# Kernel optimization log

Measured on AMD Instinct MI355X. Metric: run time of the kernel, lower is better.

Reference implementation:

```python
import jax, jax.numpy as jnp
import numpy as np

TEMPERATURE = 0.1
NEG_INF = -1e9
EPS = 1e-12

def setup_inputs() -> dict:
    key = jax.random.key(0)
    k1, k2, k3 = jax.random.split(key, 3)
    B, C, H, W = 8, 256, 128, 128
    num_classes = 150
    features = jax.random.normal(k1, (B, C, H, W), dtype=jnp.float32)
    labels = jax.random.randint(k2, (B, H, W), 0, num_classes, dtype=jnp.int32)
    text_embeddings = jax.random.normal(k3, (num_classes, C), dtype=jnp.float32)
    return {"features": features, "labels": labels, "text_embeddings": text_embeddings, "ignore_index": 255}

def _l2_normalize(x, axis=-1):
    n = jnp.linalg.norm(x, axis=axis, keepdims=True)
    return x / jnp.maximum(n, EPS)

def reference(features, labels, text_embeddings, ignore_index):
    num_classes, C = text_embeddings.shape
    B = features.shape[0]
    # [B,C,H,W] -> [B*H*W, C]
    f = jnp.transpose(features, (0, 2, 3, 1)).reshape(-1, C)
    lab = jnp.where(labels == ignore_index, 0, labels).reshape(-1)
    # segment-mean per class (fused scatter-add instead of per-class loop)
    sums = jax.ops.segment_sum(f, lab, num_segments=num_classes)          # [K,C]
    counts = jax.ops.segment_sum(jnp.ones_like(lab, dtype=f.dtype), lab, num_segments=num_classes)  # [K]
    valid = counts > 0
    prototypes = jnp.where(valid[:, None], sums / jnp.maximum(counts, 1.0)[:, None], 0.0)
    prototypes = _l2_normalize(prototypes)
    text_n = _l2_normalize(text_embeddings)
    sim = (prototypes @ text_n.T) / TEMPERATURE                            # [K,K]
    # cross-entropy restricted to valid rows/cols with identity soft targets
    masked = jnp.where(valid[None, :], sim, NEG_INF)                       # mask invalid cols
    logp = jax.nn.log_softmax(masked, axis=-1)
    diag = jnp.diagonal(logp)
    per_row = jnp.where(valid, -diag, 0.0)
    n_valid = jnp.sum(valid.astype(f.dtype))
    loss = jnp.sum(per_row) / jnp.maximum(n_valid, 1.0)
    return jnp.where(n_valid > 1, loss, 0.0)
```

## Files before the change

### kernel.cpp

```cpp
#include <hip/hip_runtime.h>
#include <math.h>

#define EPSV 1e-12f

typedef __attribute__((ext_vector_type(8))) short short8;
typedef __attribute__((ext_vector_type(4))) float f32x4;

constexpr int MT    = 10;
constexpr int K_PAD = 160;
constexpr int CPB   = 64;
constexpr int CHPX  = 64;
constexpr int PBPX  = 1024;
constexpr int NCHK  = PBPX / CHPX;
constexpr int NPB   = 128;
constexpr int THR   = 512;

__global__ __launch_bounds__(THR, 4) void protomm_kernel(
    const float* __restrict__ feat,
    const int*   __restrict__ labels,
    const int*   __restrict__ ign_p,
    float*       __restrict__ partial,
    float*       __restrict__ vmask,
    int C, int HW)
{
    __shared__ float stage[4][4096];
    __shared__ int   labL[PBPX];
    __shared__ unsigned char pres[K_PAD];

    const int tid   = threadIdx.x;
    const int w     = tid >> 6;
    const int lane  = tid & 63;
    const int rowid = lane & 15;
    const int g     = lane >> 4;
    const int ctg   = w & 1;
    const int mg    = w >> 1;

    const int bid = blockIdx.x;
    const int cg  = bid & 3;
    const int pb  = bid >> 2;
    const int b   = pb >> 4;
    const int px0 = (pb & 15) * PBPX;
    const int ig  = *ign_p;

    if (cg == 0)
        for (int i = tid; i < K_PAD; i += THR) pres[i] = 0;
    {
        int l0 = labels[(size_t)b * HW + px0 + tid];
        int l1 = labels[(size_t)b * HW + px0 + THR + tid];
        labL[tid]       = (l0 == ig) ? 0 : l0;
        labL[tid + THR] = (l1 == ig) ? 0 : l1;
    }
    __syncthreads();
    if (cg == 0) {
        int la = labL[tid];
        if ((unsigned)la < (unsigned)K_PAD) pres[la] = 1;
        la = labL[tid + THR];
        if ((unsigned)la < (unsigned)K_PAD) pres[la] = 1;
    }

    const int sch = tid >> 4;
    const int p40 = (tid & 15) ^ (sch & 7);
    const float* gb0 = feat + ((size_t)(b * C + cg * CPB + sch)) * HW + px0 + 4 * p40;
    const float* gb1 = gb0 + (size_t)32 * HW;

    auto ISSUE = [&](int ck) {
        const int buf = ck & 3;
        __builtin_amdgcn_global_load_lds(
            (const __attribute__((address_space(1))) void*)(gb0 + ck * CHPX),
            (__attribute__((address_space(3))) void*)&stage[buf][tid * 4], 16, 0, 0);
        __builtin_amdgcn_global_load_lds(
            (const __attribute__((address_space(1))) void*)(gb1 + ck * CHPX),
            (__attribute__((address_space(3))) void*)&stage[buf][tid * 4 + 2048], 16, 0, 0);
    };

    f32x4 acc0[3], acc1[3];
    #pragma unroll
    for (int j = 0; j < 3; ++j) {
        acc0[j] = (f32x4){0.f, 0.f, 0.f, 0.f};
        acc1[j] = (f32x4){0.f, 0.f, 0.f, 0.f};
    }

    auto CONSUME = [&](int ck) {
        const int buf = ck & 3;
        #pragma unroll
        for (int ks = 0; ks < 2; ++ks) {
            const int pxb = ck * CHPX + ks * 32 + g * 8;
            const int4 lA = *reinterpret_cast<const int4*>(&labL[pxb]);
            const int4 lB = *reinterpret_cast<const int4*>(&labL[pxb + 4]);
            const int px4 = ks * 8 + g * 2;
            short8 bfr0, bfr1;
            {
                const int ch = ctg * 32 + rowid;
                const int x  = ch & 7;
                const float4 f0 = *reinterpret_cast<const float4*>(
                    &stage[buf][(ch * 16 + (px4 ^ x)) * 4]);
                const float4 f1 = *reinterpret_cast<const float4*>(
                    &stage[buf][(ch * 16 + ((px4 + 1) ^ x)) * 4]);
                unsigned q0, q1, q2, q3;
                asm("v_cvt_pk_bf16_f32 %0, %1, %2" : "=v"(q0) : "v"(f0.x), "v"(f0.y));
                asm("v_cvt_pk_bf16_f32 %0, %1, %2" : "=v"(q1) : "v"(f0.z), "v"(f0.w));
                asm("v_cvt_pk_bf16_f32 %0, %1, %2" : "=v"(q2) : "v"(f1.x), "v"(f1.y));
                asm("v_cvt_pk_bf16_f32 %0, %1, %2" : "=v"(q3) : "v"(f1.z), "v"(f1.w));
                bfr0 = __builtin_bit_cast(short8, make_uint4(q0, q1, q2, q3));
            }
            {
                const int ch = ctg * 32 + 16 + rowid;
                const int x  = ch & 7;
                const float4 f0 = *reinterpret_cast<const float4*>(
                    &stage[buf][(ch * 16 + (px4 ^ x)) * 4]);
                const float4 f1 = *reinterpret_cast<const float4*>(
                    &stage[buf][(ch * 16 + ((px4 + 1) ^ x)) * 4]);
                unsigned q0, q1, q2, q3;
                asm("v_cvt_pk_bf16_f32 %0, %1, %2" : "=v"(q0) : "v"(f0.x), "v"(f0.y));
                asm("v_cvt_pk_bf16_f32 %0, %1, %2" : "=v"(q1) : "v"(f0.z), "v"(f0.w));
                asm("v_cvt_pk_bf16_f32 %0, %1, %2" : "=v"(q2) : "v"(f1.x), "v"(f1.y));
                asm("v_cvt_pk_bf16_f32 %0, %1, %2" : "=v"(q3) : "v"(f1.z), "v"(f1.w));
                bfr1 = __builtin_bit_cast(short8, make_uint4(q0, q1, q2, q3));
            }
            #pragma unroll
            for (int j = 0; j < 3; ++j) {
                const int m = mg + 4 * j;
                if (m < MT) {
                    const int tgt = m * 16 + rowid;
                    unsigned a0 = (lA.x == tgt ? 0x3F80u : 0u) | (lA.y == tgt ? 0x3F800000u : 0u);
                    unsigned a1 = (lA.z == tgt ? 0x3F80u : 0u) | (lA.w == tgt ? 0x3F800000u : 0u);
                    unsigned a2 = (lB.x == tgt ? 0x3F80u : 0u) | (lB.y == tgt ? 0x3F800000u : 0u);
                    unsigned a3 = (lB.z == tgt ? 0x3F80u : 0u) | (lB.w == tgt ? 0x3F800000u : 0u);
                    short8 afrag = __builtin_bit_cast(short8, make_uint4(a0, a1, a2, a3));
                    acc0[j] = __builtin_amdgcn_mfma_f32_16x16x32_bf16(afrag, bfr0, acc0[j], 0, 0, 0);
                    acc1[j] = __builtin_amdgcn_mfma_f32_16x16x32_bf16(afrag, bfr1, acc1[j], 0, 0, 0);
                }
            }
        }
    };

    ISSUE(0); ISSUE(1); ISSUE(2);
    #pragma unroll 1
    for (int ck = 0; ck < NCHK - 2; ++ck) {
        asm volatile("s_waitcnt vmcnt(4)" ::: "memory");
        __builtin_amdgcn_sched_barrier(0);
        __builtin_amdgcn_s_barrier();
        __builtin_amdgcn_sched_barrier(0);
        if (ck + 3 < NCHK) ISSUE(ck + 3);
        CONSUME(ck);
    }
    asm volatile("s_waitcnt vmcnt(2)" ::: "memory");
    __builtin_amdgcn_sched_barrier(0);
    __builtin_amdgcn_s_barrier();
    __builtin_amdgcn_sched_barrier(0);
    CONSUME(NCHK - 2);
    asm volatile("s_waitcnt vmcnt(0)" ::: "memory");
    __builtin_amdgcn_sched_barrier(0);
    __builtin_amdgcn_s_barrier();
    __builtin_amdgcn_sched_barrier(0);
    CONSUME(NCHK - 1);

    {
        float* dst = partial + (size_t)pb * K_PAD * C + cg * CPB;
        #pragma unroll
        for (int j = 0; j < 3; ++j) {
            const int m = mg + 4 * j;
            if (m < MT) {
                #pragma unroll
                for (int c2 = 0; c2 < 2; ++c2) {
                    const int col = (ctg * 2 + c2) * 16 + rowid;
                    #pragma unroll
                    for (int r = 0; r < 4; ++r) {
                        const int cls = m * 16 + g * 4 + r;
                        dst[(size_t)cls * C + col] = (c2 == 0) ? acc0[j][r] : acc1[j][r];
                    }
                }
            }
        }
    }
    if (cg == 0) {
        __syncthreads();
        for (int i = tid; i < K_PAD; i += THR)
            if (pres[i]) vmask[i] = 1.0f;
    }
}

__global__ __launch_bounds__(256) void tail_kernel(
    const float* __restrict__ partial,
    const float* __restrict__ text,
    const float* __restrict__ vmask,
    float* __restrict__ loss_acc,
    unsigned int* __restrict__ ticket,
    float* __restrict__ out,
    int K, int C, int nblocks)
{
    __shared__ float ph[256];
    __shared__ float scr[4][260];
    __shared__ float vm[K_PAD];
    __shared__ float red[5];
    __shared__ float wred[12];
    __shared__ unsigned int lastflag;

    const int k    = blockIdx.x;
    const int tid  = threadIdx.x;
    const int wid  = tid >> 6;
    const int lane = tid & 63;

    if (tid < K_PAD) vm[tid] = vmask[tid];
    __syncthreads();
    const bool valid = (vm[k] > 0.f);

    float contrib = 0.f;
    if (valid) {
        const int cq = tid & 63;
        const int sg = tid >> 6;
        const size_t gs = (size_t)K_PAD * C;
        const float* pbase = partial + (size_t)k * C + 4 * cq;
        float4 a0 = {0,0,0,0}, a1 = {0,0,0,0}, a2 = {0,0,0,0}, a3 = {0,0,0,0};
        float4 a4 = {0,0,0,0}, a5 = {0,0,0,0}, a6 = {0,0,0,0}, a7 = {0,0,0,0};
        for (int o = 0; o < NPB; o += 32) {
            a0 += *(const float4*)(pbase + (size_t)(o + sg +  0) * gs);
            a1 += *(const float4*)(pbase + (size_t)(o + sg +  4) * gs);
            a2 += *(const float4*)(pbase + (size_t)(o + sg +  8) * gs);
            a3 += *(const float4*)(pbase + (size_t)(o + sg + 12) * gs);
            a4 += *(const float4*)(pbase + (size_t)(o + sg + 16) * gs);
            a5 += *(const float4*)(pbase + (size_t)(o + sg + 20) * gs);
            a6 += *(const float4*)(pbase + (size_t)(o + sg + 24) * gs);
            a7 += *(const float4*)(pbase + (size_t)(o + sg + 28) * gs);
        }
        float4 asum = (((a0 + a1) + (a2 + a3)) + ((a4 + a5) + (a6 + a7)));
        *(float4*)&scr[sg][4 * cq] = asum;
        __syncthreads();
        float val = scr[0][tid] + scr[1][tid] + scr[2][tid] + scr[3][tid];

        float v = val * val;
        #pragma unroll
        for (int o = 32; o > 0; o >>= 1) v += __shfl_down(v, o);
        if (lane == 0) red[wid] = v;
        __syncthreads();
        if (tid == 0) {
            float s = red[0] + red[1] + red[2] + red[3];
            red[4] = 1.0f / fmaxf(sqrtf(s), EPSV);
        }
        __syncthreads();
        ph[tid] = val * red[4];
        __syncthreads();

        const float4 pv = *(const float4*)&ph[4 * lane];
        float m = -INFINITY, s = 0.f, skk = 0.f;
        #pragma unroll 1
        for (int gq = 0; gq < K_PAD / 16; ++gq) {
            const int j0 = gq * 16 + wid * 4;
            const float4* t0 = (const float4*)(text + (size_t)(j0 + 0 < K ? j0 + 0 : 0) * C);
            const float4* t1 = (const float4*)(text + (size_t)(j0 + 1 < K ? j0 + 1 : 0) * C);
            const float4* t2 = (const float4*)(text + (size_t)(j0 + 2 < K ? j0 + 2 : 0) * C);
            const float4* t3 = (const float4*)(text + (size_t)(j0 + 3 < K ? j0 + 3 : 0) * C);
            float4 x0 = t0[lane], x1 = t1[lane], x2 = t2[lane], x3 = t3[lane];
            float d0 = pv.x*x0.x + pv.y*x0.y + pv.z*x0.z + pv.w*x0.w;
            float q0 = x0.x*x0.x + x0.y*x0.y + x0.z*x0.z + x0.w*x0.w;
            float d1 = pv.x*x1.x + pv.y*x1.y + pv.z*x1.z + pv.w*x1.w;
            float q1 = x1.x*x1.x + x1.y*x1.y + x1.z*x1.z + x1.w*x1.w;
            float d2 = pv.x*x2.x + pv.y*x2.y + pv.z*x2.z + pv.w*x2.w;
            float q2 = x2.x*x2.x + x2.y*x2.y + x2.z*x2.z + x2.w*x2.w;
            float d3 = pv.x*x3.x + pv.y*x3.y + pv.z*x3.z + pv.w*x3.w;
            float q3 = x3.x*x3.x + x3.y*x3.y + x3.z*x3.z + x3.w*x3.w;
            #pragma unroll
            for (int o = 32; o > 0; o >>= 1) {
                d0 += __shfl_down(d0, o); d1 += __shfl_down(d1, o);
                d2 += __shfl_down(d2, o); d3 += __shfl_down(d3, o);
                q0 += __shfl_down(q0, o); q1 += __shfl_down(q1, o);
                q2 += __shfl_down(q2, o); q3 += __shfl_down(q3, o);
            }
            if (lane == 0) {
                float dd[4] = {d0, d1, d2, d3};
                float qq[4] = {q0, q1, q2, q3};
                #pragma unroll
                for (int r = 0; r < 4; ++r) {
                    int j = j0 + r;
                    float vmj = vm[j];
                    float sim = dd[r] * (10.0f / fmaxf(sqrtf(qq[r]), EPSV));
                    float ms  = vmj * sim - (1.f - vmj) * 1e9f;
                    if (j == k) skk = ms;
                    if (ms > m) { s = s * __expf(m - ms) + 1.f; m = ms; }
                    else        { s += __expf(ms - m); }
                }
            }
        }
        if (lane == 0) { wred[wid*3+0] = m; wred[wid*3+1] = s; wred[wid*3+2] = skk; }
        __syncthreads();
        if (tid == 0) {
            float M = fmaxf(fmaxf(wred[0], wred[3]), fmaxf(wred[6], wred[9]));
            float S = 0.f, SKK = 0.f;
            #pragma unroll
            for (int ww = 0; ww < 4; ++ww) {
                S   += wred[ww*3+1] * __expf(wred[ww*3+0] - M);
                SKK += wred[ww*3+2];
            }
            contrib = M + logf(S) - SKK;
        }
    }

    if (tid == 0) {
        if (valid) atomicAdd(loss_acc, contrib);
        __threadfence();
        unsigned old = atomicAdd(ticket, 1u);
        lastflag = (old == (unsigned)(nblocks - 1)) ? 1u : 0u;
    }
    __syncthreads();
    if (lastflag) {
        float v = (tid < K_PAD) ? vm[tid] : 0.f;
        #pragma unroll
        for (int o = 32; o > 0; o >>= 1) v += __shfl_down(v, o);
        if (lane == 0) red[wid] = v;
        __syncthreads();
        if (tid == 0) {
            float nv = red[0] + red[1] + red[2] + red[3];
            float total = atomicAdd(loss_acc, 0.0f);
            out[0] = (nv > 1.f) ? total / fmaxf(nv, 1.f) : 0.f;
        }
    }
}

extern "C" void kernel_launch(void* const* d_in, const int* in_sizes, int n_in,
                              void* d_out, int out_size, void* d_ws, size_t ws_size,
                              hipStream_t stream) {
    const float* feat   = (const float*)d_in[0];
    const int*   labels = (const int*)d_in[1];
    const float* text   = (const float*)d_in[2];
    const int*   ign    = (const int*)d_in[3];

    const int B  = 8;
    const int N  = in_sizes[1];
    const int HW = N / B;
    const int C  = in_sizes[0] / N;
    const int K  = in_sizes[2] / C;

    float*        partial  = (float*)d_ws;
    float*        vmask    = partial + (size_t)NPB * K_PAD * C;
    float*        loss_acc = vmask + K_PAD;
    unsigned int* ticket   = (unsigned int*)(loss_acc + 1);

    hipMemsetAsync(vmask, 0, (K_PAD + 2) * sizeof(float), stream);

    protomm_kernel<<<NPB * 4, THR, 0, stream>>>(
        feat, labels, ign, partial, vmask, C, HW);

    tail_kernel<<<K, 256, 0, stream>>>(
        partial, text, vmask, loss_acc, ticket, (float*)d_out, K, C, K);
}
```

Measured before the change: 71.38 us.

## Split channels into eight groups and stage partial tiles through LDS

Each block now handles 32 channels instead of 64, so the grid doubles to 1024 blocks and the LDS staging buffer halves, which the new launch bounds use to aim for higher occupancy. Each wave keeps one accumulator set and issues one global-to-LDS load per chunk. The partial-sum output is rewritten as a contiguous per-block tile: results go to LDS first and are then written with coalesced float4 stores. The tail kernel's indexing is updated to this layout. In exchange, label loading and one-hot fragment construction are repeated across twice as many blocks, and two extra barriers are added in the epilogue.

New measurement: 70.97 us. About the same (-0.6%).

```diff
diff --git a/kernel.cpp b/kernel.cpp
--- a/kernel.cpp
+++ b/kernel.cpp
@@ -8,14 +8,15 @@
 
 constexpr int MT    = 10;
 constexpr int K_PAD = 160;
-constexpr int CPB   = 64;
+constexpr int CPB   = 32;
+constexpr int CG    = 8;
 constexpr int CHPX  = 64;
 constexpr int PBPX  = 1024;
 constexpr int NCHK  = PBPX / CHPX;
 constexpr int NPB   = 128;
 constexpr int THR   = 512;
 
-__global__ __launch_bounds__(THR, 4) void protomm_kernel(
+__global__ __launch_bounds__(THR, 8) void protomm_kernel(
     const float* __restrict__ feat,
     const int*   __restrict__ labels,
     const int*   __restrict__ ign_p,
@@ -23,7 +24,7 @@
     float*       __restrict__ vmask,
     int C, int HW)
 {
-    __shared__ float stage[4][4096];
+    __shared__ float stage[4][2048];
     __shared__ int   labL[PBPX];
     __shared__ unsigned char pres[K_PAD];
 
@@ -32,12 +33,12 @@
     const int lane  = tid & 63;
     const int rowid = lane & 15;
     const int g     = lane >> 4;
-    const int ctg   = w & 1;
+    const int ct    = w & 1;
     const int mg    = w >> 1;
 
     const int bid = blockIdx.x;
-    const int cg  = bid & 3;
-    const int pb  = bid >> 2;
+    const int cg  = bid & 7;
+    const int pb  = bid >> 3;
     const int b   = pb >> 4;
     const int px0 = (pb & 15) * PBPX;
     const int ig  = *ign_p;
@@ -60,25 +61,18 @@
 
     const int sch = tid >> 4;
     const int p40 = (tid & 15) ^ (sch & 7);
-    const float* gb0 = feat + ((size_t)(b * C + cg * CPB + sch)) * HW + px0 + 4 * p40;
-    const float* gb1 = gb0 + (size_t)32 * HW;
+    const float* gb = feat + ((size_t)(b * C + cg * CPB + sch)) * HW + px0 + 4 * p40;
 
     auto ISSUE = [&](int ck) {
         const int buf = ck & 3;
         __builtin_amdgcn_global_load_lds(
-            (const __attribute__((address_space(1))) void*)(gb0 + ck * CHPX),
+            (const __attribute__((address_space(1))) void*)(gb + ck * CHPX),
             (__attribute__((address_space(3))) void*)&stage[buf][tid * 4], 16, 0, 0);
-        __builtin_amdgcn_global_load_lds(
-            (const __attribute__((address_space(1))) void*)(gb1 + ck * CHPX),
-            (__attribute__((address_space(3))) void*)&stage[buf][tid * 4 + 2048], 16, 0, 0);
     };
 
-    f32x4 acc0[3], acc1[3];
+    f32x4 acc[3];
     #pragma unroll
-    for (int j = 0; j < 3; ++j) {
-        acc0[j] = (f32x4){0.f, 0.f, 0.f, 0.f};
-        acc1[j] = (f32x4){0.f, 0.f, 0.f, 0.f};
-    }
+    for (int j = 0; j < 3; ++j) acc[j] = (f32x4){0.f, 0.f, 0.f, 0.f};
 
     auto CONSUME = [&](int ck) {
         const int buf = ck & 3;
@@ -88,35 +82,18 @@
             const int4 lA = *reinterpret_cast<const int4*>(&labL[pxb]);
             const int4 lB = *reinterpret_cast<const int4*>(&labL[pxb + 4]);
             const int px4 = ks * 8 + g * 2;
-            short8 bfr0, bfr1;
-            {
-                const int ch = ctg * 32 + rowid;
-                const int x  = ch & 7;
-                const float4 f0 = *reinterpret_cast<const float4*>(
-                    &stage[buf][(ch * 16 + (px4 ^ x)) * 4]);
-                const float4 f1 = *reinterpret_cast<const float4*>(
-                    &stage[buf][(ch * 16 + ((px4 + 1) ^ x)) * 4]);
-                unsigned q0, q1, q2, q3;
-                asm("v_cvt_pk_bf16_f32 %0, %1, %2" : "=v"(q0) : "v"(f0.x), "v"(f0.y));
-                asm("v_cvt_pk_bf16_f32 %0, %1, %2" : "=v"(q1) : "v"(f0.z), "v"(f0.w));
-                asm("v_cvt_pk_bf16_f32 %0, %1, %2" : "=v"(q2) : "v"(f1.x), "v"(f1.y));
-                asm("v_cvt_pk_bf16_f32 %0, %1, %2" : "=v"(q3) : "v"(f1.z), "v"(f1.w));
-                bfr0 = __builtin_bit_cast(short8, make_uint4(q0, q1, q2, q3));
-            }
-            {
-                const int ch = ctg * 32 + 16 + rowid;
-                const int x  = ch & 7;
-                const float4 f0 = *reinterpret_cast<const float4*>(
-                    &stage[buf][(ch * 16 + (px4 ^ x)) * 4]);
-                const float4 f1 = *reinterpret_cast<const float4*>(
-                    &stage[buf][(ch * 16 + ((px4 + 1) ^ x)) * 4]);
-                unsigned q0, q1, q2, q3;
-                asm("v_cvt_pk_bf16_f32 %0, %1, %2" : "=v"(q0) : "v"(f0.x), "v"(f0.y));
-                asm("v_cvt_pk_bf16_f32 %0, %1, %2" : "=v"(q1) : "v"(f0.z), "v"(f0.w));
-                asm("v_cvt_pk_bf16_f32 %0, %1, %2" : "=v"(q2) : "v"(f1.x), "v"(f1.y));
-                asm("v_cvt_pk_bf16_f32 %0, %1, %2" : "=v"(q3) : "v"(f1.z), "v"(f1.w));
-                bfr1 = __builtin_bit_cast(short8, make_uint4(q0, q1, q2, q3));
-            }
+            const int ch  = ct * 16 + rowid;
+            const int x   = ch & 7;
+            const float4 f0 = *reinterpret_cast<const float4*>(
+                &stage[buf][(ch * 16 + (px4 ^ x)) * 4]);
+            const float4 f1 = *reinterpret_cast<const float4*>(
+                &stage[buf][(ch * 16 + ((px4 + 1) ^ x)) * 4]);
+            unsigned q0, q1, q2, q3;
+            asm("v_cvt_pk_bf16_f32 %0, %1, %2" : "=v"(q0) : "v"(f0.x), "v"(f0.y));
+            asm("v_cvt_pk_bf16_f32 %0, %1, %2" : "=v"(q1) : "v"(f0.z), "v"(f0.w));
+            asm("v_cvt_pk_bf16_f32 %0, %1, %2" : "=v"(q2) : "v"(f1.x), "v"(f1.y));
+            asm("v_cvt_pk_bf16_f32 %0, %1, %2" : "=v"(q3) : "v"(f1.z), "v"(f1.w));
+            const short8 bfrag = __builtin_bit_cast(short8, make_uint4(q0, q1, q2, q3));
             #pragma unroll
             for (int j = 0; j < 3; ++j) {
                 const int m = mg + 4 * j;
@@ -127,8 +104,7 @@
                     unsigned a2 = (lB.x == tgt ? 0x3F80u : 0u) | (lB.y == tgt ? 0x3F800000u : 0u);
                     unsigned a3 = (lB.z == tgt ? 0x3F80u : 0u) | (lB.w == tgt ? 0x3F800000u : 0u);
                     short8 afrag = __builtin_bit_cast(short8, make_uint4(a0, a1, a2, a3));
-                    acc0[j] = __builtin_amdgcn_mfma_f32_16x16x32_bf16(afrag, bfr0, acc0[j], 0, 0, 0);
-                    acc1[j] = __builtin_amdgcn_mfma_f32_16x16x32_bf16(afrag, bfr1, acc1[j], 0, 0, 0);
+                    acc[j] = __builtin_amdgcn_mfma_f32_16x16x32_bf16(afrag, bfrag, acc[j], 0, 0, 0);
                 }
             }
         }
@@ -137,44 +113,49 @@
     ISSUE(0); ISSUE(1); ISSUE(2);
     #pragma unroll 1
     for (int ck = 0; ck < NCHK - 2; ++ck) {
-        asm volatile("s_waitcnt vmcnt(4)" ::: "memory");
+        asm volatile("s_waitcnt vmcnt(2) lgkmcnt(0)" ::: "memory");
         __builtin_amdgcn_sched_barrier(0);
         __builtin_amdgcn_s_barrier();
         __builtin_amdgcn_sched_barrier(0);
         if (ck + 3 < NCHK) ISSUE(ck + 3);
         CONSUME(ck);
     }
-    asm volatile("s_waitcnt vmcnt(2)" ::: "memory");
+    asm volatile("s_waitcnt vmcnt(1) lgkmcnt(0)" ::: "memory");
     __builtin_amdgcn_sched_barrier(0);
     __builtin_amdgcn_s_barrier();
     __builtin_amdgcn_sched_barrier(0);
     CONSUME(NCHK - 2);
-    asm volatile("s_waitcnt vmcnt(0)" ::: "memory");
+    asm volatile("s_waitcnt vmcnt(0) lgkmcnt(0)" ::: "memory");
     __builtin_amdgcn_sched_barrier(0);
     __builtin_amdgcn_s_barrier();
     __builtin_amdgcn_sched_barrier(0);
     CONSUME(NCHK - 1);
 
+    __syncthreads();
     {
-        float* dst = partial + (size_t)pb * K_PAD * C + cg * CPB;
+        float* ftile = &stage[0][0];
         #pragma unroll
         for (int j = 0; j < 3; ++j) {
             const int m = mg + 4 * j;
             if (m < MT) {
                 #pragma unroll
-                for (int c2 = 0; c2 < 2; ++c2) {
-                    const int col = (ctg * 2 + c2) * 16 + rowid;
-                    #pragma unroll
-                    for (int r = 0; r < 4; ++r) {
-                        const int cls = m * 16 + g * 4 + r;
-                        dst[(size_t)cls * C + col] = (c2 == 0) ? acc0[j][r] : acc1[j][r];
-                    }
-                }
-            }
+                for (int r = 0; r < 4; ++r)
+                    ftile[(m * 16 + g * 4 + r) * CPB + ct * 16 + rowid] = acc[j][r];
+            }
+        }
+    }
+    __syncthreads();
+    {
+        const float4* src = reinterpret_cast<const float4*>(&stage[0][0]);
+        float4* dst = reinterpret_cast<float4*>(
+            partial + ((size_t)pb * CG + cg) * (size_t)K_PAD * CPB);
+        #pragma unroll
+        for (int i = 0; i < (K_PAD * CPB / 4 + THR - 1) / THR; ++i) {
+            int idx = tid + i * THR;
+            if (idx < K_PAD * CPB / 4) dst[idx] = src[idx];
         }
     }
     if (cg == 0) {
-        __syncthreads();
         for (int i = tid; i < K_PAD; i += THR)
             if (pres[i]) vmask[i] = 1.0f;
     }
@@ -209,8 +190,9 @@
     if (valid) {
         const int cq = tid & 63;
         const int sg = tid >> 6;
-        const size_t gs = (size_t)K_PAD * C;
-        const float* pbase = partial + (size_t)k * C + 4 * cq;
+        const size_t gs = (size_t)CG * K_PAD * CPB;
+        const float* pbase = partial
+            + ((size_t)(cq >> 3) * K_PAD + k) * CPB + 4 * (cq & 7);
         float4 a0 = {0,0,0,0}, a1 = {0,0,0,0}, a2 = {0,0,0,0}, a3 = {0,0,0,0};
         float4 a4 = {0,0,0,0}, a5 = {0,0,0,0}, a6 = {0,0,0,0}, a7 = {0,0,0,0};
         for (int o = 0; o < NPB; o += 32) {
@@ -331,13 +313,13 @@
     const int K  = in_sizes[2] / C;
 
     float*        partial  = (float*)d_ws;
-    float*        vmask    = partial + (size_t)NPB * K_PAD * C;
+    float*        vmask    = partial + (size_t)NPB * CG * K_PAD * CPB;
     float*        loss_acc = vmask + K_PAD;
     unsigned int* ticket   = (unsigned int*)(loss_acc + 1);
 
     hipMemsetAsync(vmask, 0, (K_PAD + 2) * sizeof(float), stream);
 
-    protomm_kernel<<<NPB * 4, THR, 0, stream>>>(
+    protomm_kernel<<<NPB * CG, THR, 0, stream>>>(
         feat, labels, ign, partial, vmask, C, HW);
 
     tail_kernel<<<K, 256, 0, stream>>>(
```

## Prefetch features into registers and convert to bf16 once before LDS staging

Applied to the files above, without the earlier changes.

Replaces the four-deep global_load_lds pipeline of fp32 64-pixel chunks with register prefetch of 256-pixel chunks. Each chunk is converted to bf16 once and written into a padded, double-buffered LDS tile, and the MFMA loop reads bf16 fragments directly. This halves LDS footprint per chunk, removes duplicated conversion work, and cuts the number of barriers per block. In exchange it holds the prefetch in registers (pressure at 4 blocks/CU), keeps only one chunk of prefetch in flight, and adds a second barrier per iteration.

Result: faster. 68.33 us (-4.3%).

```diff
diff --git a/kernel.cpp b/kernel.cpp
--- a/kernel.cpp
+++ b/kernel.cpp
@@ -9,11 +9,13 @@
 constexpr int MT    = 10;
 constexpr int K_PAD = 160;
 constexpr int CPB   = 64;
-constexpr int CHPX  = 64;
+constexpr int CGN   = 4;
+constexpr int CHPX  = 256;
 constexpr int PBPX  = 1024;
 constexpr int NCHK  = PBPX / CHPX;
 constexpr int NPB   = 128;
 constexpr int THR   = 512;
+constexpr int LROW  = 264;
 
 __global__ __launch_bounds__(THR, 4) void protomm_kernel(
     const float* __restrict__ feat,
@@ -23,7 +25,7 @@
     float*       __restrict__ vmask,
     int C, int HW)
 {
-    __shared__ float stage[4][4096];
+    __shared__ unsigned short Bf[2][CPB * LROW];
     __shared__ int   labL[PBPX];
     __shared__ unsigned char pres[K_PAD];
 
@@ -42,6 +44,17 @@
     const int px0 = (pb & 15) * PBPX;
     const int ig  = *ign_p;
 
+    const float* fbase = feat + ((size_t)b * C + cg * CPB + w) * HW + px0 + 4 * lane;
+
+    float4 pf[8];
+    auto ISSUE = [&](int ck) {
+        #pragma unroll
+        for (int i = 0; i < 8; ++i)
+            pf[i] = *reinterpret_cast<const float4*>(fbase + (size_t)(8 * i) * HW + ck * CHPX);
+    };
+
+    ISSUE(0);
+
     if (cg == 0)
         for (int i = tid; i < K_PAD; i += THR) pres[i] = 0;
     {
@@ -58,21 +71,6 @@
         if ((unsigned)la < (unsigned)K_PAD) pres[la] = 1;
     }
 
-    const int sch = tid >> 4;
-    const int p40 = (tid & 15) ^ (sch & 7);
-    const float* gb0 = feat + ((size_t)(b * C + cg * CPB + sch)) * HW + px0 + 4 * p40;
-    const float* gb1 = gb0 + (size_t)32 * HW;
-
-    auto ISSUE = [&](int ck) {
-        const int buf = ck & 3;
-        __builtin_amdgcn_global_load_lds(
-            (const __attribute__((address_space(1))) void*)(gb0 + ck * CHPX),
-            (__attribute__((address_space(3))) void*)&stage[buf][tid * 4], 16, 0, 0);
-        __builtin_amdgcn_global_load_lds(
-            (const __attribute__((address_space(1))) void*)(gb1 + ck * CHPX),
-            (__attribute__((address_space(3))) void*)&stage[buf][tid * 4 + 2048], 16, 0, 0);
-    };
-
     f32x4 acc0[3], acc1[3];
     #pragma unroll
     for (int j = 0; j < 3; ++j) {
@@ -80,43 +78,27 @@
         acc1[j] = (f32x4){0.f, 0.f, 0.f, 0.f};
     }
 
-    auto CONSUME = [&](int ck) {
-        const int buf = ck & 3;
-        #pragma unroll
-        for (int ks = 0; ks < 2; ++ks) {
+    auto COMMIT = [&](int buf) {
+        #pragma unroll
+        for (int i = 0; i < 8; ++i) {
+            unsigned u0, u1;
+            asm("v_cvt_pk_bf16_f32 %0, %1, %2" : "=v"(u0) : "v"(pf[i].x), "v"(pf[i].y));
+            asm("v_cvt_pk_bf16_f32 %0, %1, %2" : "=v"(u1) : "v"(pf[i].z), "v"(pf[i].w));
+            *reinterpret_cast<uint2*>(&Bf[buf][(w + 8 * i) * LROW + 4 * lane]) =
+                make_uint2(u0, u1);
+        }
+    };
+
+    auto CONSUME = [&](int buf, int ck) {
+        #pragma unroll
+        for (int ks = 0; ks < CHPX / 32; ++ks) {
             const int pxb = ck * CHPX + ks * 32 + g * 8;
             const int4 lA = *reinterpret_cast<const int4*>(&labL[pxb]);
             const int4 lB = *reinterpret_cast<const int4*>(&labL[pxb + 4]);
-            const int px4 = ks * 8 + g * 2;
-            short8 bfr0, bfr1;
-            {
-                const int ch = ctg * 32 + rowid;
-                const int x  = ch & 7;
-                const float4 f0 = *reinterpret_cast<const float4*>(
-                    &stage[buf][(ch * 16 + (px4 ^ x)) * 4]);
-                const float4 f1 = *reinterpret_cast<const float4*>(
-                    &stage[buf][(ch * 16 + ((px4 + 1) ^ x)) * 4]);
-                unsigned q0, q1, q2, q3;
-                asm("v_cvt_pk_bf16_f32 %0, %1, %2" : "=v"(q0) : "v"(f0.x), "v"(f0.y));
-                asm("v_cvt_pk_bf16_f32 %0, %1, %2" : "=v"(q1) : "v"(f0.z), "v"(f0.w));
-                asm("v_cvt_pk_bf16_f32 %0, %1, %2" : "=v"(q2) : "v"(f1.x), "v"(f1.y));
-                asm("v_cvt_pk_bf16_f32 %0, %1, %2" : "=v"(q3) : "v"(f1.z), "v"(f1.w));
-                bfr0 = __builtin_bit_cast(short8, make_uint4(q0, q1, q2, q3));
-            }
-            {
-                const int ch = ctg * 32 + 16 + rowid;
-                const int x  = ch & 7;
-                const float4 f0 = *reinterpret_cast<const float4*>(
-                    &stage[buf][(ch * 16 + (px4 ^ x)) * 4]);
-                const float4 f1 = *reinterpret_cast<const float4*>(
-                    &stage[buf][(ch * 16 + ((px4 + 1) ^ x)) * 4]);
-                unsigned q0, q1, q2, q3;
-                asm("v_cvt_pk_bf16_f32 %0, %1, %2" : "=v"(q0) : "v"(f0.x), "v"(f0.y));
-                asm("v_cvt_pk_bf16_f32 %0, %1, %2" : "=v"(q1) : "v"(f0.z), "v"(f0.w));
-                asm("v_cvt_pk_bf16_f32 %0, %1, %2" : "=v"(q2) : "v"(f1.x), "v"(f1.y));
-                asm("v_cvt_pk_bf16_f32 %0, %1, %2" : "=v"(q3) : "v"(f1.z), "v"(f1.w));
-                bfr1 = __builtin_bit_cast(short8, make_uint4(q0, q1, q2, q3));
-            }
+            const short8 bf0 = *reinterpret_cast<const short8*>(
+                &Bf[buf][((2 * ctg + 0) * 16 + rowid) * LROW + ks * 32 + g * 8]);
+            const short8 bf1 = *reinterpret_cast<const short8*>(
+                &Bf[buf][((2 * ctg + 1) * 16 + rowid) * LROW + ks * 32 + g * 8]);
             #pragma unroll
             for (int j = 0; j < 3; ++j) {
                 const int m = mg + 4 * j;
@@ -127,33 +109,27 @@
                     unsigned a2 = (lB.x == tgt ? 0x3F80u : 0u) | (lB.y == tgt ? 0x3F800000u : 0u);
                     unsigned a3 = (lB.z == tgt ? 0x3F80u : 0u) | (lB.w == tgt ? 0x3F800000u : 0u);
                     short8 afrag = __builtin_bit_cast(short8, make_uint4(a0, a1, a2, a3));
-                    acc0[j] = __builtin_amdgcn_mfma_f32_16x16x32_bf16(afrag, bfr0, acc0[j], 0, 0, 0);
-                    acc1[j] = __builtin_amdgcn_mfma_f32_16x16x32_bf16(afrag, bfr1, acc1[j], 0, 0, 0);
+                    acc0[j] = __builtin_amdgcn_mfma_f32_16x16x32_bf16(afrag, bf0, acc0[j], 0, 0, 0);
+                    acc1[j] = __builtin_amdgcn_mfma_f32_16x16x32_bf16(afrag, bf1, acc1[j], 0, 0, 0);
                 }
             }
         }
     };
 
-    ISSUE(0); ISSUE(1); ISSUE(2);
     #pragma unroll 1
-    for (int ck = 0; ck < NCHK - 2; ++ck) {
-        asm volatile("s_waitcnt vmcnt(4)" ::: "memory");
+    for (int ck = 0; ck < NCHK; ++ck) {
+        const int cur = ck & 1;
+        COMMIT(cur);
+        if (ck + 1 < NCHK) ISSUE(ck + 1);
+        asm volatile("s_waitcnt lgkmcnt(0)" ::: "memory");
         __builtin_amdgcn_sched_barrier(0);
         __builtin_amdgcn_s_barrier();
         __builtin_amdgcn_sched_barrier(0);
-        if (ck + 3 < NCHK) ISSUE(ck + 3);
-        CONSUME(ck);
-    }
-    asm volatile("s_waitcnt vmcnt(2)" ::: "memory");
-    __builtin_amdgcn_sched_barrier(0);
-    __builtin_amdgcn_s_barrier();
-    __builtin_amdgcn_sched_barrier(0);
-    CONSUME(NCHK - 2);
-    asm volatile("s_waitcnt vmcnt(0)" ::: "memory");
-    __builtin_amdgcn_sched_barrier(0);
-    __builtin_amdgcn_s_barrier();
-    __builtin_amdgcn_sched_barrier(0);
-    CONSUME(NCHK - 1);
+        CONSUME(cur, ck);
+        __builtin_amdgcn_sched_barrier(0);
+        __builtin_amdgcn_s_barrier();
+        __builtin_amdgcn_sched_barrier(0);
+    }
 
     {
         float* dst = partial + (size_t)pb * K_PAD * C + cg * CPB;
@@ -162,22 +138,17 @@
             const int m = mg + 4 * j;
             if (m < MT) {
                 #pragma unroll
-                for (int c2 = 0; c2 < 2; ++c2) {
-                    const int col = (ctg * 2 + c2) * 16 + rowid;
-                    #pragma unroll
-                    for (int r = 0; r < 4; ++r) {
-                        const int cls = m * 16 + g * 4 + r;
-                        dst[(size_t)cls * C + col] = (c2 == 0) ? acc0[j][r] : acc1[j][r];
-                    }
+                for (int r = 0; r < 4; ++r) {
+                    const int cls = m * 16 + g * 4 + r;
+                    dst[(size_t)cls * C + (2 * ctg + 0) * 16 + rowid] = acc0[j][r];
+                    dst[(size_t)cls * C + (2 * ctg + 1) * 16 + rowid] = acc1[j][r];
                 }
             }
         }
     }
-    if (cg == 0) {
-        __syncthreads();
+    if (cg == 0)
         for (int i = tid; i < K_PAD; i += THR)
             if (pres[i]) vmask[i] = 1.0f;
-    }
 }
 
 __global__ __launch_bounds__(256) void tail_kernel(
@@ -337,7 +308,7 @@
 
     hipMemsetAsync(vmask, 0, (K_PAD + 2) * sizeof(float), stream);
 
-    protomm_kernel<<<NPB * 4, THR, 0, stream>>>(
+    protomm_kernel<<<NPB * CGN, THR, 0, stream>>>(
         feat, labels, ign, partial, vmask, C, HW);
 
     tail_kernel<<<K, 256, 0, stream>>>(
```
